# Performance work log

Hardware: AMD Instinct MI355X
Metric: run time of the kernel (lower is better)

The kernel has to match this reference:

```python
import jax, jax.numpy as jnp
import numpy as np

BZ, C_IN, C_OUT, N, T, KT = 16, 3, 64, 307, 24, 3


def setup_inputs() -> dict:
    key = jax.random.key(0)
    ks = jax.random.split(key, 16)
    rn = lambda i, sh, s=1.0: jax.random.normal(ks[i], sh, dtype=jnp.float32) * s
    return {
        "x": rn(0, (BZ, C_IN, N, T)),
        "supports": rn(1, (N, N)),  # adjacency scores; entries > 0 define edges
        "conv1_w": rn(2, (C_OUT, C_IN), 0.1),
        "conv1_b": jnp.zeros((C_OUT,), jnp.float32),
        "time_w": rn(3, (C_OUT, C_IN, 1, KT), 0.1),
        "time_b": jnp.zeros((C_OUT,), jnp.float32),
        "W1": rn(4, (C_OUT, C_OUT), 0.1), "a1s": rn(5, (C_OUT,), 0.1), "a1d": rn(6, (C_OUT,), 0.1),
        "W2": rn(7, (C_OUT, C_OUT), 0.1), "a2s": rn(8, (C_OUT,), 0.1), "a2d": rn(9, (C_OUT,), 0.1),
        "t1w": rn(10, (C_OUT,), 0.1),
        "t2w": rn(11, (N,), 0.1),
        "tw": rn(12, (N, C_OUT), 0.1),
        "tb": jnp.zeros((T, T), jnp.float32),
        "tv": rn(13, (T, T), 0.1),
        "bn_g": jnp.ones((T,), jnp.float32), "bn_b": jnp.zeros((T,), jnp.float32),
        "ln_w": jnp.ones((C_OUT, N, T), jnp.float32), "ln_b": jnp.zeros((C_OUT, N, T), jnp.float32),
    }


def _lrelu(z, s=0.01):
    return jnp.where(z > 0, z, s * z)


def _gat(x, adj, W, a_src, a_dst, slope=0.3):
    # x: [B, C, N, T] -> per-time-step single-head graph attention masked by adj > 0
    h = jnp.einsum('bcnt,cf->btnf', x, W)                      # [B,T,N,F]
    e = (jnp.einsum('btnf,f->btn', h, a_src)[:, :, :, None]
         + jnp.einsum('btnf,f->btn', h, a_dst)[:, :, None, :])  # [B,T,N,N]
    e = _lrelu(e, slope)
    e = jnp.where(adj[None, None] > 0, e, -9e15)
    att = jax.nn.softmax(e, axis=-1)
    out = jnp.einsum('btnm,btmf->btnf', att, h)
    return out.transpose(0, 3, 2, 1), att                      # [B,F,N,T], [B,T,N,N]


def _forward(x, supports, conv1_w, conv1_b, time_w, time_b,
             W1, a1s, a1d, W2, a2s, a2d,
             t1w, t2w, tw, tb, tv, bn_g, bn_b, ln_w, ln_b):
    # residual branch: 1x1 conv
    x_input = jnp.einsum('bcnt,oc->bont', x, conv1_w) + conv1_b[None, :, None, None]
    # temporal conv (1, Kt), padding (0, 1)
    x1 = jax.lax.conv_general_dilated(
        x, time_w, (1, 1), [(0, 0), (1, 1)],
        dimension_numbers=('NCHW', 'OIHW', 'NCHW')) + time_b[None, :, None, None]
    x1 = _lrelu(x1)  # dropout is identity in eval
    # two dynamic GATs: filter + gate
    filt, S_coef = _gat(x1, supports, W1, a1s, a1d)
    gate, _ = _gat(x1, supports, W2, a2s, a2d)
    x1 = jax.nn.sigmoid(gate) * _lrelu(filt)
    # ---- TATT_1 temporal attention ----
    f1 = jnp.einsum('bcnt,c->btn', x1, t1w)   # conv1 (C->1) on [B,C,T,N]
    f2 = jnp.einsum('bcnt,n->bct', x1, t2w)   # conv2 (N->1) on [B,N,C,T]
    logits = jax.nn.sigmoid(jnp.einsum('btn,nc,bcq->btq', f1, tw, f2) + tb)
    logits = jnp.einsum('pt,btq->bpq', tv, logits)
    # BatchNorm1d in eval (running_mean=0, running_var=1), channels = last dim after transpose
    lg = logits.transpose(0, 2, 1)
    lg = lg / np.sqrt(1.0 + 1e-5).astype(np.float32) * bn_g[None, :, None] + bn_b[None, :, None]
    logits = lg.transpose(0, 2, 1)
    # global B mask: causal mask over time steps
    Bmask = jnp.where(jnp.tril(jnp.ones((T, T), jnp.float32)) > 0, 0.0, -1e13)
    coefs = jax.nn.softmax(logits + Bmask, axis=-1)
    T_coef = coefs.transpose(0, 2, 1)
    # combine over time + residual + LayerNorm over [C, N, T]
    x1 = jnp.einsum('bcnl,blq->bcnq', x1, T_coef)
    y = _lrelu(x1) + x_input
    mu = jnp.mean(y, axis=(1, 2, 3), keepdims=True)
    var = jnp.var(y, axis=(1, 2, 3), keepdims=True)
    out = (y - mu) / jnp.sqrt(var + 1e-5) * ln_w[None] + ln_b[None]
    return out, S_coef, T_coef


def reference(x, supports, conv1_w, conv1_b, time_w, time_b,
              W1, a1s, a1d, W2, a2s, a2d,
              t1w, t2w, tw, tb, tv, bn_g, bn_b, ln_w, ln_b):
    return _forward(x, supports, conv1_w, conv1_b, time_w, time_b,
                    W1, a1s, a1d, W2, a2s, a2d,
                    t1w, t2w, tw, tb, tv, bn_g, bn_b, ln_w, ln_b)
```

## Files before the change

kernel.cpp:

```cpp
#include <hip/hip_runtime.h>

typedef unsigned short u16;
typedef unsigned int u32;
typedef __attribute__((ext_vector_type(8))) short bf16x8;
typedef __attribute__((ext_vector_type(4))) float f32x4;

#define BZ 16
#define CIN 3
#define C 64
#define N_ 307
#define T_ 24
#define BT (BZ*T_)
#define ROWS (BT*N_)
#define CNT (C*N_*T_)

#define OUT_ELEMS 7544832
#define S_ELEMS   36191616

#define HSTRIDE 344

__device__ __forceinline__ u16 f2b(float v) {
    union { float f; unsigned u; } x; x.f = v;
    unsigned u = x.u;
    unsigned rb = (u >> 16) & 1u;
    u += 0x7fffu + rb;
    return (u16)(u >> 16);
}
__device__ __forceinline__ float wave_sum(float v) {
#pragma unroll
    for (int m = 32; m > 0; m >>= 1) v += __shfl_xor(v, m);
    return v;
}

__global__ __launch_bounds__(512) void kAdjPre(const float* __restrict__ sup,
        u32* __restrict__ adjm)
{
    int idx = blockIdx.x*512 + threadIdx.x;
    if (idx >= 3200) return;
    int n = idx / 10, kw = idx - n*10;
    u32 bits = 0;
    if (n < N_) {
        const float* row = sup + n*N_ + kw*32;
        int lim = N_ - kw*32; if (lim > 32) lim = 32;
        for (int j = 0; j < lim; ++j)
            if (row[j] > 0.f) bits |= (1u << j);
    }
    adjm[idx] = bits;
}

template<int G>
__global__ __launch_bounds__(512, 2) void kGAT(
        const float* __restrict__ x, const float* __restrict__ sup,
        const float* __restrict__ tmw, const float* __restrict__ tmb,
        const float* __restrict__ W, const float* __restrict__ asp,
        const float* __restrict__ adp,
        const float* __restrict__ t1w, const float* __restrict__ t2w,
        const u32* __restrict__ adjm,
        float* __restrict__ agbuf, float* __restrict__ f1,
        float* __restrict__ f2)
{
    __shared__ u16 sHT[64*HSTRIDE];
    __shared__ float sX[3200];
    __shared__ float sTmw[576];
    __shared__ float sTmb[64];
    __shared__ float sU[64];
    __shared__ float sV[64];
    __shared__ float sHs[320];
    __shared__ float sHd[320];
    __shared__ float sF2[8*64];

    int bt = blockIdx.x;
    int b = bt / T_, t = bt - b * T_;
    int tid = threadIdx.x;
    int w = tid >> 6, lane = tid & 63;
    int l15 = lane & 15, quad = lane >> 4;

    for (int i = tid; i < 3*320*3; i += 512) {
        int k = i % 3; int rest = i / 3;
        int n = rest % 320; int ci = rest / 320;
        int tt = t - 1 + k;
        float v = 0.f;
        if (n < N_ && tt >= 0 && tt < T_)
            v = x[((b*CIN + ci)*N_ + n)*T_ + tt];
        sX[i] = v;
    }
    for (int i = tid; i < 576; i += 512) sTmw[i] = tmw[i];
    if (tid < 64) {
        sTmb[tid] = tmb[tid];
        float u = 0.f, v = 0.f;
#pragma unroll
        for (int f4 = 0; f4 < 16; ++f4) {
            float4 wr = ((const float4*)(W + tid*64))[f4];
            float4 s4 = ((const float4*)asp)[f4];
            float4 d4 = ((const float4*)adp)[f4];
            u += wr.x*s4.x + wr.y*s4.y + wr.z*s4.z + wr.w*s4.w;
            v += wr.x*d4.x + wr.y*d4.y + wr.z*d4.z + wr.w*d4.w;
        }
        sU[tid] = u; sV[tid] = v;
    }

    bf16x8 wf[2][4];
#pragma unroll
    for (int kk = 0; kk < 2; ++kk)
#pragma unroll
    for (int nt = 0; nt < 4; ++nt) {
        bf16x8 a;
#pragma unroll
        for (int j = 0; j < 8; ++j)
            a[j] = (short)f2b(W[(kk*32 + quad*8 + j)*64 + nt*16 + l15]);
        wf[kk][nt] = a;
    }
    __syncthreads();

#pragma unroll 1
    for (int mt = w; mt < 20; mt += 8) {
        int row = mt*16 + l15;
        float xt[16];
#pragma unroll
        for (int half = 0; half < 2; ++half) {
#pragma unroll
            for (int j = 0; j < 8; ++j) {
                int c = half*32 + quad*8 + j;
                float acc = sTmb[c];
#pragma unroll
                for (int ci = 0; ci < 3; ++ci) {
                    const float* xr = &sX[(ci*320 + row)*3];
                    const float* wr = &sTmw[(c*3 + ci)*3];
                    acc += wr[0]*xr[0] + wr[1]*xr[1] + wr[2]*xr[2];
                }
                xt[half*8 + j] = acc > 0.f ? acc : 0.01f*acc;
            }
        }
        float ps = 0.f, pd = 0.f;
#pragma unroll
        for (int j = 0; j < 8; ++j) {
            ps += xt[j]*sU[quad*8 + j] + xt[8 + j]*sU[32 + quad*8 + j];
            pd += xt[j]*sV[quad*8 + j] + xt[8 + j]*sV[32 + quad*8 + j];
        }
        ps += __shfl_xor(ps, 16); ps += __shfl_xor(ps, 32);
        pd += __shfl_xor(pd, 16); pd += __shfl_xor(pd, 32);
        if (quad == 0 && row < N_) { sHs[row] = ps; sHd[row] = pd; }
        bf16x8 a0, a1;
#pragma unroll
        for (int j = 0; j < 8; ++j) {
            a0[j] = (short)f2b(xt[j]);
            a1[j] = (short)f2b(xt[8 + j]);
        }
        f32x4 hacc[4];
#pragma unroll
        for (int nt = 0; nt < 4; ++nt) {
            f32x4 z = {0.f, 0.f, 0.f, 0.f};
            z = __builtin_amdgcn_mfma_f32_16x16x32_bf16(a0, wf[0][nt], z, 0, 0, 0);
            z = __builtin_amdgcn_mfma_f32_16x16x32_bf16(a1, wf[1][nt], z, 0, 0, 0);
            hacc[nt] = z;
        }
#pragma unroll
        for (int nt = 0; nt < 4; ++nt)
#pragma unroll
        for (int reg = 0; reg < 4; ++reg)
            sHT[(nt*16 + l15)*HSTRIDE + mt*16 + quad*4 + reg] = f2b(hacc[nt][reg]);
    }
    if (tid < 13) { sHs[307+tid] = -700.f; sHd[307+tid] = -700.f; }
    __syncthreads();

    u32* sAdj = (u32*)sX;
    for (int i = tid; i < 3200; i += 512) sAdj[i] = adjm[i];
    __syncthreads();

    float t1all[4];
    if (G == 1) {
#pragma unroll
        for (int nt = 0; nt < 4; ++nt) t1all[nt] = t1w[nt*16 + l15];
    }
    float q[4] = {0,0,0,0};

#pragma unroll 1
    for (int mt = w; mt < 20; mt += 8) {
        int n = mt*16 + l15;
        float hsv = sHs[n];
        float asum = 0.f;
        bf16x8 af[10];
#pragma unroll
        for (int ks = 0; ks < 10; ++ks) {
            u32 aw = sAdj[n*10 + ks] >> (quad*8);
            int m0 = ks*32 + quad*8;
            bf16x8 a;
#pragma unroll
            for (int j = 0; j < 8; ++j) {
                float e = hsv + sHd[m0 + j];
                e = e > 0.f ? e : 0.3f*e;
                float ww = ((aw >> j) & 1u) ? __expf(e) : 0.f;
                asum += ww;
                a[j] = (short)f2b(ww);
            }
            af[ks] = a;
        }
        asum += __shfl_xor(asum, 16);
        asum += __shfl_xor(asum, 32);
        float invv = (asum > 0.f) ? 1.f/asum : 0.f;

        float p[4] = {0,0,0,0};
#pragma unroll 1
        for (int nt = 0; nt < 4; ++nt) {
            f32x4 acc = {0.f, 0.f, 0.f, 0.f};
            const u16* bbase = sHT + (nt*16 + l15)*HSTRIDE;
#pragma unroll
            for (int ks = 0; ks < 10; ++ks) {
                bf16x8 bfrag = *(const bf16x8*)(bbase + ks*32 + quad*8);
                acc = __builtin_amdgcn_mfma_f32_16x16x32_bf16(af[ks], bfrag, acc, 0, 0, 0);
            }
            int c = nt*16 + l15;
#pragma unroll
            for (int reg = 0; reg < 4; ++reg) {
                int n2 = mt*16 + quad*4 + reg;
                float inv2 = __shfl(invv, quad*4 + reg);
                float a = acc[reg] * inv2;
                size_t idx = (size_t)(bt*N_ + n2)*64 + c;
                if (G == 0) {
                    if (n2 < N_) agbuf[idx] = a;
                } else {
                    float a1 = (n2 < N_) ? agbuf[idx] : 0.f;
                    float gt = 1.f / (1.f + __expf(-a));
                    float fv = a1 > 0.f ? a1 : 0.01f*a1;
                    float xv = gt * fv;
                    if (n2 < N_) agbuf[idx] = xv; else xv = 0.f;
                    p[reg] += xv * t1all[nt];
                    float t2v = (n2 < N_) ? t2w[n2] : 0.f;
                    q[nt] += xv * t2v;
                }
            }
        }
        if (G == 1) {
#pragma unroll
            for (int reg = 0; reg < 4; ++reg) {
                float s = p[reg];
                s += __shfl_xor(s, 1); s += __shfl_xor(s, 2);
                s += __shfl_xor(s, 4); s += __shfl_xor(s, 8);
                int n2 = mt*16 + quad*4 + reg;
                if (l15 == 0 && n2 < N_) f1[bt*N_ + n2] = s;
            }
        }
    }
    if (G == 1) {
#pragma unroll
        for (int nt = 0; nt < 4; ++nt) {
            float s = q[nt];
            s += __shfl_xor(s, 16); s += __shfl_xor(s, 32);
            if (quad == 0) sF2[w*64 + nt*16 + l15] = s;
        }
        __syncthreads();
        if (tid < 64) {
            float s = sF2[tid];
#pragma unroll
            for (int ww = 1; ww < 8; ++ww) s += sF2[ww*64 + tid];
            f2[(b*C + tid)*T_ + t] = s;
        }
    }
}

__global__ __launch_bounds__(512) void kSc(
        const float* __restrict__ x, const float* __restrict__ sup,
        const float* __restrict__ tmw, const float* __restrict__ tmb,
        const float* __restrict__ W, const float* __restrict__ asp,
        const float* __restrict__ adp, float* __restrict__ Sc)
{
    __shared__ float sHs[320];
    __shared__ float sHd[320];
    __shared__ float sU[64], sV[64];
    __shared__ float sTmw[576];
    __shared__ float sTmb[64];

    int half = blockIdx.x;
    int bt = blockIdx.y;
    int b = bt / T_, t = bt - b * T_;
    int tid = threadIdx.x;
    int w = tid >> 6, lane = tid & 63;

    for (int i = tid; i < 576; i += 512) sTmw[i] = tmw[i];
    if (tid < 64) {
        sTmb[tid] = tmb[tid];
        float u = 0.f, v = 0.f;
#pragma unroll
        for (int f4 = 0; f4 < 16; ++f4) {
            float4 wr = ((const float4*)(W + tid*64))[f4];
            float4 s4 = ((const float4*)asp)[f4];
            float4 d4 = ((const float4*)adp)[f4];
            u += wr.x*s4.x + wr.y*s4.y + wr.z*s4.z + wr.w*s4.w;
            v += wr.x*d4.x + wr.y*d4.y + wr.z*d4.z + wr.w*d4.w;
        }
        sU[tid] = u; sV[tid] = v;
    }
    __syncthreads();

    if (tid < 320) {
        int n = tid;
        if (n >= N_) { sHs[n] = -700.f; sHd[n] = -700.f; }
        else {
            float xv[3][3];
#pragma unroll
            for (int ci = 0; ci < 3; ++ci) {
                const float* xp = x + ((b*CIN + ci)*N_ + n)*T_ + t;
                xv[ci][0] = (t > 0)      ? xp[-1] : 0.f;
                xv[ci][1] = xp[0];
                xv[ci][2] = (t < T_ - 1) ? xp[1]  : 0.f;
            }
            float hs = 0.f, hd = 0.f;
#pragma unroll
            for (int c = 0; c < 64; ++c) {
                float acc = sTmb[c];
#pragma unroll
                for (int ci = 0; ci < 3; ++ci) {
                    const float* wr = &sTmw[(c*3 + ci)*3];
                    acc += wr[0]*xv[ci][0] + wr[1]*xv[ci][1] + wr[2]*xv[ci][2];
                }
                float xt = acc > 0.f ? acc : 0.01f*acc;
                hs += xt * sU[c];
                hd += xt * sV[c];
            }
            sHs[n] = hs; sHd[n] = hd;
        }
    }
    __syncthreads();

    int base = half ? 154 : 0;
    int cnt  = half ? 153 : 154;
#pragma unroll 1
    for (int r = w; r < cnt; r += 8) {
        int n = base + r;
        float hsv = sHs[n];
        const float* srow = sup + n*N_;
        float ww0, ww1, ww2, ww3, ww4;
        {
            float e;
            ww0 = 0.f;
            if (srow[lane] > 0.f) { e = hsv + sHd[lane]; e = e > 0.f ? e : 0.3f*e; ww0 = __expf(e); }
            ww1 = 0.f;
            if (srow[64 + lane] > 0.f) { e = hsv + sHd[64 + lane]; e = e > 0.f ? e : 0.3f*e; ww1 = __expf(e); }
            ww2 = 0.f;
            if (srow[128 + lane] > 0.f) { e = hsv + sHd[128 + lane]; e = e > 0.f ? e : 0.3f*e; ww2 = __expf(e); }
            ww3 = 0.f;
            if (srow[192 + lane] > 0.f) { e = hsv + sHd[192 + lane]; e = e > 0.f ? e : 0.3f*e; ww3 = __expf(e); }
            ww4 = 0.f;
            if (256 + lane < N_ && srow[256 + lane] > 0.f) {
                e = hsv + sHd[256 + lane]; e = e > 0.f ? e : 0.3f*e; ww4 = __expf(e);
            }
        }
        float asum = wave_sum(ww0 + ww1 + ww2 + ww3 + ww4);
        float inv = (asum > 0.f) ? 1.f/asum : 0.f;
        float* drow = Sc + (size_t)(bt*N_ + n)*N_;
        drow[lane]       = ww0*inv;
        drow[64 + lane]  = ww1*inv;
        drow[128 + lane] = ww2*inv;
        drow[192 + lane] = ww3*inv;
        if (256 + lane < N_) drow[256 + lane] = ww4*inv;
    }
}

__global__ __launch_bounds__(256) void kD0(const float* __restrict__ f1,
        const float* __restrict__ tw, float* __restrict__ g1)
{
    __shared__ float part[4][64];
    int bt = blockIdx.x;
    int w = threadIdx.x >> 6, lane = threadIdx.x & 63;
    float acc = 0.f;
    for (int n = w*77; n < (w+1)*77 && n < N_; ++n)
        acc += f1[bt*N_ + n] * tw[n*64 + lane];
    part[w][lane] = acc;
    __syncthreads();
    if (threadIdx.x < 64) {
        float s = part[0][threadIdx.x] + part[1][threadIdx.x]
                + part[2][threadIdx.x] + part[3][threadIdx.x];
        g1[bt*64 + threadIdx.x] = s;
    }
}

__global__ __launch_bounds__(256) void kD(const float* __restrict__ g1,
        const float* __restrict__ f2, const float* __restrict__ tb,
        const float* __restrict__ tv,
        const float* __restrict__ bng, const float* __restrict__ bnb,
        float* __restrict__ coefs, float* __restrict__ Tc,
        float* __restrict__ stats)
{
    __shared__ float g1s[T_][C];
    __shared__ float f2s[C][T_];
    __shared__ float lg[T_][T_];
    __shared__ float l2[T_][T_];
    int b = blockIdx.x, tid = threadIdx.x;
    if (tid == 0) { stats[2*b] = 0.f; stats[2*b + 1] = 0.f; }
    for (int idx = tid; idx < T_*C; idx += 256) {
        int t = idx / C, c = idx - t*C;
        g1s[t][c] = g1[(b*T_ + t)*C + c];
        int c2 = idx / T_, t2 = idx - c2*T_;
        f2s[c2][t2] = f2[(b*C + c2)*T_ + t2];
    }
    __syncthreads();
    for (int idx = tid; idx < T_*T_; idx += 256) {
        int t = idx / T_, q = idx - t*T_;
        float s = 0.f;
#pragma unroll
        for (int c = 0; c < C; ++c) s += g1s[t][c] * f2s[c][q];
        s += tb[t*T_ + q];
        lg[t][q] = 1.f / (1.f + expf(-s));
    }
    __syncthreads();
    const float bnscale = 0.99999500003749972f;
    for (int idx = tid; idx < T_*T_; idx += 256) {
        int p = idx / T_, q = idx - p*T_;
        float s = 0.f;
#pragma unroll
        for (int t = 0; t < T_; ++t) s += tv[p*T_ + t] * lg[t][q];
        s = s * bnscale * bng[q] + bnb[q];
        if (q > p) s += -1e13f;
        l2[p][q] = s;
    }
    __syncthreads();
    if (tid < T_) {
        int p = tid;
        float mx = -3e38f;
#pragma unroll
        for (int q = 0; q < T_; ++q) mx = fmaxf(mx, l2[p][q]);
        float e[T_]; float sum = 0.f;
#pragma unroll
        for (int q = 0; q < T_; ++q) { e[q] = expf(l2[p][q] - mx); sum += e[q]; }
        float inv = 1.f / sum;
#pragma unroll
        for (int q = 0; q < T_; ++q) {
            float v = e[q] * inv;
            coefs[(b*T_ + p)*T_ + q] = v;
            Tc[(b*T_ + q)*T_ + p] = v;
        }
    }
}

__device__ __forceinline__ void compute_y(int b, int n, int lane,
        const float* __restrict__ xg, const float cf[T_][T_],
        const float* __restrict__ x, const float* __restrict__ c1w,
        const float* __restrict__ c1b, float* y)
{
    float acc[T_];
#pragma unroll
    for (int q = 0; q < T_; ++q) acc[q] = 0.f;
#pragma unroll 1
    for (int l = 0; l < T_; ++l) {
        float xv = xg[(size_t)((b*T_ + l)*N_ + n)*64 + lane];
#pragma unroll
        for (int q = 0; q < T_; ++q) acc[q] += xv * cf[q][l];
    }
    float w0 = c1w[lane*3+0], w1 = c1w[lane*3+1], w2 = c1w[lane*3+2];
    float bb = c1b[lane];
    const float* xb0 = x + ((b*CIN + 0)*N_ + n)*T_;
    const float* xb1 = x + ((b*CIN + 1)*N_ + n)*T_;
    const float* xb2 = x + ((b*CIN + 2)*N_ + n)*T_;
#pragma unroll
    for (int q = 0; q < T_; ++q) {
        float xin = bb + w0*xb0[q] + w1*xb1[q] + w2*xb2[q];
        float v = acc[q];
        v = v > 0.f ? v : 0.01f*v;
        y[q] = v + xin;
    }
}

__global__ __launch_bounds__(256) void kE1(const float* __restrict__ xg,
        const float* __restrict__ coefs, const float* __restrict__ x,
        const float* __restrict__ c1w, const float* __restrict__ c1b,
        float* __restrict__ stats)
{
    __shared__ float cf[T_][T_];
    int b = blockIdx.y;
    for (int i = threadIdx.x; i < T_*T_; i += 256) ((float*)cf)[i] = coefs[b*T_*T_ + i];
    __syncthreads();
    int w = threadIdx.x >> 6, lane = threadIdx.x & 63;
    int n = blockIdx.x*4 + w;
    if (n >= N_) return;
    float y[T_];
    compute_y(b, n, lane, xg, cf, x, c1w, c1b, y);
    float s = 0.f, ss = 0.f;
#pragma unroll
    for (int q = 0; q < T_; ++q) { s += y[q]; ss += y[q]*y[q]; }
    s = wave_sum(s); ss = wave_sum(ss);
    if (lane == 0) { atomicAdd(&stats[2*b], s); atomicAdd(&stats[2*b + 1], ss); }
}

__global__ __launch_bounds__(256) void kE2(const float* __restrict__ xg,
        const float* __restrict__ coefs, const float* __restrict__ x,
        const float* __restrict__ c1w, const float* __restrict__ c1b,
        const float* __restrict__ stats, const float* __restrict__ lnw,
        const float* __restrict__ lnb, float* __restrict__ out)
{
    __shared__ float cf[T_][T_];
    int b = blockIdx.y;
    for (int i = threadIdx.x; i < T_*T_; i += 256) ((float*)cf)[i] = coefs[b*T_*T_ + i];
    __syncthreads();
    int w = threadIdx.x >> 6, lane = threadIdx.x & 63;
    int n = blockIdx.x*4 + w;
    if (n >= N_) return;
    float y[T_];
    compute_y(b, n, lane, xg, cf, x, c1w, c1b, y);
    float mu   = stats[2*b] * (1.f/CNT);
    float var  = stats[2*b + 1] * (1.f/CNT) - mu*mu;
    float rstd = rsqrtf(fmaxf(var, 0.f) + 1e-5f);
    int gi = (lane*N_ + n)*T_;
    float ov[T_];
#pragma unroll
    for (int q = 0; q < T_; ++q)
        ov[q] = (y[q] - mu)*rstd*lnw[gi + q] + lnb[gi + q];
    float* dst = out + ((size_t)(b*C + lane)*N_ + n)*T_;
#pragma unroll
    for (int j = 0; j < 6; ++j) {
        float4 v;
        v.x = ov[j*4+0]; v.y = ov[j*4+1]; v.z = ov[j*4+2]; v.w = ov[j*4+3];
        ((float4*)dst)[j] = v;
    }
}

extern "C" void kernel_launch(void* const* d_in, const int* in_sizes, int n_in,
                              void* d_out, int out_size, void* d_ws, size_t ws_size,
                              hipStream_t stream)
{
    const float* x   = (const float*)d_in[0];
    const float* sup = (const float*)d_in[1];
    const float* c1w = (const float*)d_in[2];
    const float* c1b = (const float*)d_in[3];
    const float* tmw = (const float*)d_in[4];
    const float* tmb = (const float*)d_in[5];
    const float* W1  = (const float*)d_in[6];
    const float* a1s = (const float*)d_in[7];
    const float* a1d = (const float*)d_in[8];
    const float* W2  = (const float*)d_in[9];
    const float* a2s = (const float*)d_in[10];
    const float* a2d = (const float*)d_in[11];
    const float* t1w = (const float*)d_in[12];
    const float* t2w = (const float*)d_in[13];
    const float* tw  = (const float*)d_in[14];
    const float* tb  = (const float*)d_in[15];
    const float* tv  = (const float*)d_in[16];
    const float* bng = (const float*)d_in[17];
    const float* bnb = (const float*)d_in[18];
    const float* lnw = (const float*)d_in[19];
    const float* lnb = (const float*)d_in[20];

    float* out = (float*)d_out;
    float* Sc  = out + OUT_ELEMS;
    float* Tc  = Sc + (size_t)S_ELEMS;

    float* agbuf = Sc;
    float* f1    = Sc + (size_t)OUT_ELEMS;
    float* f2    = f1 + ROWS;
    float* g1    = f2 + BZ*C*T_;
    float* coefs = g1 + BT*C;
    float* stats = coefs + BZ*T_*T_;
    u32*   adjm  = (u32*)(stats + 32);

    kAdjPre<<<7, 512, 0, stream>>>(sup, adjm);
    kGAT<0><<<BT, 512, 0, stream>>>(x, sup, tmw, tmb, W1, a1s, a1d,
                                    t1w, t2w, adjm, agbuf, f1, f2);
    kGAT<1><<<BT, 512, 0, stream>>>(x, sup, tmw, tmb, W2, a2s, a2d,
                                    t1w, t2w, adjm, agbuf, f1, f2);
    kD0<<<BT, 256, 0, stream>>>(f1, tw, g1);
    kD<<<BZ, 256, 0, stream>>>(g1, f2, tb, tv, bng, bnb, coefs, Tc, stats);
    kE1<<<dim3(77, BZ), 256, 0, stream>>>(agbuf, coefs, x, c1w, c1b, stats);
    kE2<<<dim3(77, BZ), 256, 0, stream>>>(agbuf, coefs, x, c1w, c1b, stats, lnw, lnb, out);
    kSc<<<dim3(2, BT), 512, 0, stream>>>(x, sup, tmw, tmb, W1, a1s, a1d, Sc);
}
```

Before: 642.2 us.

## Fuse both GAT passes into one kernel keeping first-pass output in registers

Merges the two per-(b,t) GAT kernels into a single kernel. The first GAT's aggregated features stay in registers instead of being written to and reread from a global buffer. The second pass rebuilds its temporal-conv input straight from global x while the LDS slot holds the adjacency mask. The attention tile loop is also restructured to interleave weight computation with MFMAs per k-slice, and launch bounds are raised to 4 blocks per CU. The cost is higher register pressure (48 extra fp32 values per thread held across phases), with a risk of spills or lower occupancy.

```diff
diff --git a/kernel.cpp b/kernel.cpp
--- a/kernel.cpp
+++ b/kernel.cpp
@@ -48,26 +48,149 @@
     adjm[idx] = bits;
 }
 
-template<int G>
-__global__ __launch_bounds__(512, 2) void kGAT(
-        const float* __restrict__ x, const float* __restrict__ sup,
+template<int LDSX>
+__device__ __forceinline__ void phase1_core(
+        const float* __restrict__ x, const float* __restrict__ Wg,
+        const float* sXw, const float* sTmw, const float* sTmb,
+        const float* sUp, const float* sVp,
+        u16* sHTp, float* sHsp, float* sHdp,
+        int b, int t, int w, int lane)
+{
+    int l15 = lane & 15, quad = lane >> 4;
+#pragma unroll
+    for (int ti = 0; ti < 3; ++ti) {
+        int mt = w + ti*8;
+        if (mt < 20) {
+            int row = mt*16 + l15;
+            float xv[9];
+            if (LDSX) {
+#pragma unroll
+                for (int ci = 0; ci < 3; ++ci)
+#pragma unroll
+                for (int k = 0; k < 3; ++k)
+                    xv[ci*3 + k] = sXw[(ci*320 + row)*3 + k];
+            } else {
+                bool rk = row < N_;
+                int rc = rk ? row : 0;
+#pragma unroll
+                for (int ci = 0; ci < 3; ++ci) {
+                    const float* xp = x + ((b*CIN + ci)*N_ + rc)*T_ + t;
+                    xv[ci*3 + 0] = (rk && t > 0)      ? xp[-1] : 0.f;
+                    xv[ci*3 + 1] = rk                 ? xp[0]  : 0.f;
+                    xv[ci*3 + 2] = (rk && t < T_ - 1) ? xp[1]  : 0.f;
+                }
+            }
+            float xt[16];
+#pragma unroll
+            for (int half = 0; half < 2; ++half)
+#pragma unroll
+            for (int j = 0; j < 8; ++j) {
+                int c = half*32 + quad*8 + j;
+                float acc = sTmb[c];
+#pragma unroll
+                for (int ci = 0; ci < 3; ++ci) {
+                    const float* wr = &sTmw[(c*3 + ci)*3];
+                    acc += wr[0]*xv[ci*3] + wr[1]*xv[ci*3+1] + wr[2]*xv[ci*3+2];
+                }
+                xt[half*8 + j] = acc > 0.f ? acc : 0.01f*acc;
+            }
+            float ps = 0.f, pd = 0.f;
+#pragma unroll
+            for (int j = 0; j < 8; ++j) {
+                ps += xt[j]*sUp[quad*8 + j] + xt[8 + j]*sUp[32 + quad*8 + j];
+                pd += xt[j]*sVp[quad*8 + j] + xt[8 + j]*sVp[32 + quad*8 + j];
+            }
+            ps += __shfl_xor(ps, 16); ps += __shfl_xor(ps, 32);
+            pd += __shfl_xor(pd, 16); pd += __shfl_xor(pd, 32);
+            if (quad == 0 && row < N_) { sHsp[row] = ps; sHdp[row] = pd; }
+            bf16x8 a0, a1;
+#pragma unroll
+            for (int j = 0; j < 8; ++j) {
+                a0[j] = (short)f2b(xt[j]);
+                a1[j] = (short)f2b(xt[8 + j]);
+            }
+            f32x4 hacc[4];
+#pragma unroll
+            for (int nt = 0; nt < 4; ++nt) hacc[nt] = (f32x4){0.f,0.f,0.f,0.f};
+#pragma unroll
+            for (int kk = 0; kk < 2; ++kk) {
+                bf16x8 wf[4];
+#pragma unroll
+                for (int nt = 0; nt < 4; ++nt) {
+                    bf16x8 a;
+#pragma unroll
+                    for (int j = 0; j < 8; ++j)
+                        a[j] = (short)f2b(Wg[(kk*32 + quad*8 + j)*64 + nt*16 + l15]);
+                    wf[nt] = a;
+                }
+#pragma unroll
+                for (int nt = 0; nt < 4; ++nt)
+                    hacc[nt] = __builtin_amdgcn_mfma_f32_16x16x32_bf16(
+                        kk ? a1 : a0, wf[nt], hacc[nt], 0, 0, 0);
+            }
+#pragma unroll
+            for (int nt = 0; nt < 4; ++nt) {
+                u32 w0 = (u32)f2b(hacc[nt][0]) | ((u32)f2b(hacc[nt][1]) << 16);
+                u32 w1 = (u32)f2b(hacc[nt][2]) | ((u32)f2b(hacc[nt][3]) << 16);
+                u32* dst = (u32*)(sHTp + (nt*16 + l15)*HSTRIDE + mt*16 + quad*4);
+                dst[0] = w0; dst[1] = w1;
+            }
+        }
+    }
+}
+
+__device__ __forceinline__ void att_tile(
+        const u32* sAdj, const u16* sHTp, const float* sHsp, const float* sHdp,
+        int mt, int l15, int quad, f32x4 acc[4], float* invv_out)
+{
+    int n = mt*16 + l15;
+    float hsv = sHsp[n];
+    float asum = 0.f;
+#pragma unroll
+    for (int nt = 0; nt < 4; ++nt) acc[nt] = (f32x4){0.f,0.f,0.f,0.f};
+#pragma unroll
+    for (int ks = 0; ks < 10; ++ks) {
+        u32 aw = sAdj[n*10 + ks] >> (quad*8);
+        int m0 = ks*32 + quad*8;
+        bf16x8 a;
+#pragma unroll
+        for (int j = 0; j < 8; ++j) {
+            float e = hsv + sHdp[m0 + j];
+            e = e > 0.f ? e : 0.3f*e;
+            float ww = ((aw >> j) & 1u) ? __expf(e) : 0.f;
+            asum += ww;
+            a[j] = (short)f2b(ww);
+        }
+        const u16* bb = sHTp + m0;
+#pragma unroll
+        for (int nt = 0; nt < 4; ++nt) {
+            bf16x8 bfrag = *(const bf16x8*)(bb + (nt*16 + l15)*HSTRIDE);
+            acc[nt] = __builtin_amdgcn_mfma_f32_16x16x32_bf16(a, bfrag, acc[nt], 0, 0, 0);
+        }
+    }
+    asum += __shfl_xor(asum, 16);
+    asum += __shfl_xor(asum, 32);
+    *invv_out = (asum > 0.f) ? 1.f/asum : 0.f;
+}
+
+__global__ __launch_bounds__(512, 4) void kGATF(
+        const float* __restrict__ x,
         const float* __restrict__ tmw, const float* __restrict__ tmb,
-        const float* __restrict__ W, const float* __restrict__ asp,
-        const float* __restrict__ adp,
+        const float* __restrict__ W1, const float* __restrict__ a1s,
+        const float* __restrict__ a1d,
+        const float* __restrict__ W2, const float* __restrict__ a2s,
+        const float* __restrict__ a2d,
         const float* __restrict__ t1w, const float* __restrict__ t2w,
         const u32* __restrict__ adjm,
-        float* __restrict__ agbuf, float* __restrict__ f1,
+        float* __restrict__ xg, float* __restrict__ f1,
         float* __restrict__ f2)
 {
     __shared__ u16 sHT[64*HSTRIDE];
-    __shared__ float sX[3200];
+    __shared__ float sXA[3200];
     __shared__ float sTmw[576];
     __shared__ float sTmb[64];
-    __shared__ float sU[64];
-    __shared__ float sV[64];
-    __shared__ float sHs[320];
-    __shared__ float sHd[320];
-    __shared__ float sF2[8*64];
+    __shared__ float sU1[64], sV1[64], sU2[64], sV2[64];
+    __shared__ float sHs[320], sHd[320];
 
     int bt = blockIdx.x;
     int b = bt / T_, t = bt - b * T_;
@@ -75,162 +198,95 @@
     int w = tid >> 6, lane = tid & 63;
     int l15 = lane & 15, quad = lane >> 4;
 
-    for (int i = tid; i < 3*320*3; i += 512) {
+    for (int i = tid; i < 2880; i += 512) {
         int k = i % 3; int rest = i / 3;
         int n = rest % 320; int ci = rest / 320;
         int tt = t - 1 + k;
         float v = 0.f;
         if (n < N_ && tt >= 0 && tt < T_)
             v = x[((b*CIN + ci)*N_ + n)*T_ + tt];
-        sX[i] = v;
+        sXA[i] = v;
     }
     for (int i = tid; i < 576; i += 512) sTmw[i] = tmw[i];
-    if (tid < 64) {
-        sTmb[tid] = tmb[tid];
+    if (tid < 128) {
+        int c = tid & 63;
+        const float* Wp = (tid < 64) ? W1 : W2;
+        const float* sp = (tid < 64) ? a1s : a2s;
+        const float* dp = (tid < 64) ? a1d : a2d;
         float u = 0.f, v = 0.f;
 #pragma unroll
         for (int f4 = 0; f4 < 16; ++f4) {
-            float4 wr = ((const float4*)(W + tid*64))[f4];
-            float4 s4 = ((const float4*)asp)[f4];
-            float4 d4 = ((const float4*)adp)[f4];
+            float4 wr = ((const float4*)(Wp + c*64))[f4];
+            float4 s4 = ((const float4*)sp)[f4];
+            float4 d4 = ((const float4*)dp)[f4];
             u += wr.x*s4.x + wr.y*s4.y + wr.z*s4.z + wr.w*s4.w;
             v += wr.x*d4.x + wr.y*d4.y + wr.z*d4.z + wr.w*d4.w;
         }
-        sU[tid] = u; sV[tid] = v;
-    }
-
-    bf16x8 wf[2][4];
-#pragma unroll
-    for (int kk = 0; kk < 2; ++kk)
-#pragma unroll
-    for (int nt = 0; nt < 4; ++nt) {
-        bf16x8 a;
-#pragma unroll
-        for (int j = 0; j < 8; ++j)
-            a[j] = (short)f2b(W[(kk*32 + quad*8 + j)*64 + nt*16 + l15]);
-        wf[kk][nt] = a;
-    }
-    __syncthreads();
-
-#pragma unroll 1
-    for (int mt = w; mt < 20; mt += 8) {
-        int row = mt*16 + l15;
-        float xt[16];
-#pragma unroll
-        for (int half = 0; half < 2; ++half) {
-#pragma unroll
-            for (int j = 0; j < 8; ++j) {
-                int c = half*32 + quad*8 + j;
-                float acc = sTmb[c];
-#pragma unroll
-                for (int ci = 0; ci < 3; ++ci) {
-                    const float* xr = &sX[(ci*320 + row)*3];
-                    const float* wr = &sTmw[(c*3 + ci)*3];
-                    acc += wr[0]*xr[0] + wr[1]*xr[1] + wr[2]*xr[2];
-                }
-                xt[half*8 + j] = acc > 0.f ? acc : 0.01f*acc;
-            }
-        }
-        float ps = 0.f, pd = 0.f;
-#pragma unroll
-        for (int j = 0; j < 8; ++j) {
-            ps += xt[j]*sU[quad*8 + j] + xt[8 + j]*sU[32 + quad*8 + j];
-            pd += xt[j]*sV[quad*8 + j] + xt[8 + j]*sV[32 + quad*8 + j];
-        }
-        ps += __shfl_xor(ps, 16); ps += __shfl_xor(ps, 32);
-        pd += __shfl_xor(pd, 16); pd += __shfl_xor(pd, 32);
-        if (quad == 0 && row < N_) { sHs[row] = ps; sHd[row] = pd; }
-        bf16x8 a0, a1;
-#pragma unroll
-        for (int j = 0; j < 8; ++j) {
-            a0[j] = (short)f2b(xt[j]);
-            a1[j] = (short)f2b(xt[8 + j]);
-        }
-        f32x4 hacc[4];
-#pragma unroll
-        for (int nt = 0; nt < 4; ++nt) {
-            f32x4 z = {0.f, 0.f, 0.f, 0.f};
-            z = __builtin_amdgcn_mfma_f32_16x16x32_bf16(a0, wf[0][nt], z, 0, 0, 0);
-            z = __builtin_amdgcn_mfma_f32_16x16x32_bf16(a1, wf[1][nt], z, 0, 0, 0);
-            hacc[nt] = z;
-        }
-#pragma unroll
-        for (int nt = 0; nt < 4; ++nt)
-#pragma unroll
-        for (int reg = 0; reg < 4; ++reg)
-            sHT[(nt*16 + l15)*HSTRIDE + mt*16 + quad*4 + reg] = f2b(hacc[nt][reg]);
-    }
+        if (tid < 64) { sU1[c] = u; sV1[c] = v; sTmb[c] = tmb[c]; }
+        else          { sU2[c] = u; sV2[c] = v; }
+    }
+    __syncthreads();
+
+    phase1_core<1>(x, W1, sXA, sTmw, sTmb, sU1, sV1, sHT, sHs, sHd, b, t, w, lane);
     if (tid < 13) { sHs[307+tid] = -700.f; sHd[307+tid] = -700.f; }
     __syncthreads();
 
-    u32* sAdj = (u32*)sX;
+    u32* sAdj = (u32*)sXA;
     for (int i = tid; i < 3200; i += 512) sAdj[i] = adjm[i];
     __syncthreads();
 
+    float fr[3][4][4];
+#pragma unroll
+    for (int ti = 0; ti < 3; ++ti) {
+        int mt = w + ti*8;
+        if (mt < 20) {
+            f32x4 acc[4]; float invv;
+            att_tile(sAdj, sHT, sHs, sHd, mt, l15, quad, acc, &invv);
+#pragma unroll
+            for (int nt = 0; nt < 4; ++nt)
+#pragma unroll
+            for (int reg = 0; reg < 4; ++reg) {
+                float inv2 = __shfl(invv, quad*4 + reg);
+                fr[ti][nt][reg] = acc[nt][reg] * inv2;
+            }
+        }
+    }
+    __syncthreads();
+
+    phase1_core<0>(x, W2, nullptr, sTmw, sTmb, sU2, sV2, sHT, sHs, sHd, b, t, w, lane);
+    __syncthreads();
+
     float t1all[4];
-    if (G == 1) {
-#pragma unroll
-        for (int nt = 0; nt < 4; ++nt) t1all[nt] = t1w[nt*16 + l15];
-    }
+#pragma unroll
+    for (int nt = 0; nt < 4; ++nt) t1all[nt] = t1w[nt*16 + l15];
     float q[4] = {0,0,0,0};
 
-#pragma unroll 1
-    for (int mt = w; mt < 20; mt += 8) {
-        int n = mt*16 + l15;
-        float hsv = sHs[n];
-        float asum = 0.f;
-        bf16x8 af[10];
-#pragma unroll
-        for (int ks = 0; ks < 10; ++ks) {
-            u32 aw = sAdj[n*10 + ks] >> (quad*8);
-            int m0 = ks*32 + quad*8;
-            bf16x8 a;
-#pragma unroll
-            for (int j = 0; j < 8; ++j) {
-                float e = hsv + sHd[m0 + j];
-                e = e > 0.f ? e : 0.3f*e;
-                float ww = ((aw >> j) & 1u) ? __expf(e) : 0.f;
-                asum += ww;
-                a[j] = (short)f2b(ww);
-            }
-            af[ks] = a;
-        }
-        asum += __shfl_xor(asum, 16);
-        asum += __shfl_xor(asum, 32);
-        float invv = (asum > 0.f) ? 1.f/asum : 0.f;
-
-        float p[4] = {0,0,0,0};
-#pragma unroll 1
-        for (int nt = 0; nt < 4; ++nt) {
-            f32x4 acc = {0.f, 0.f, 0.f, 0.f};
-            const u16* bbase = sHT + (nt*16 + l15)*HSTRIDE;
-#pragma unroll
-            for (int ks = 0; ks < 10; ++ks) {
-                bf16x8 bfrag = *(const bf16x8*)(bbase + ks*32 + quad*8);
-                acc = __builtin_amdgcn_mfma_f32_16x16x32_bf16(af[ks], bfrag, acc, 0, 0, 0);
-            }
-            int c = nt*16 + l15;
-#pragma unroll
-            for (int reg = 0; reg < 4; ++reg) {
-                int n2 = mt*16 + quad*4 + reg;
-                float inv2 = __shfl(invv, quad*4 + reg);
-                float a = acc[reg] * inv2;
-                size_t idx = (size_t)(bt*N_ + n2)*64 + c;
-                if (G == 0) {
-                    if (n2 < N_) agbuf[idx] = a;
-                } else {
-                    float a1 = (n2 < N_) ? agbuf[idx] : 0.f;
-                    float gt = 1.f / (1.f + __expf(-a));
-                    float fv = a1 > 0.f ? a1 : 0.01f*a1;
+#pragma unroll
+    for (int ti = 0; ti < 3; ++ti) {
+        int mt = w + ti*8;
+        if (mt < 20) {
+            f32x4 acc[4]; float invv;
+            att_tile(sAdj, sHT, sHs, sHd, mt, l15, quad, acc, &invv);
+            float p[4] = {0,0,0,0};
+#pragma unroll
+            for (int nt = 0; nt < 4; ++nt) {
+                int c = nt*16 + l15;
+#pragma unroll
+                for (int reg = 0; reg < 4; ++reg) {
+                    int n2 = mt*16 + quad*4 + reg;
+                    float inv2 = __shfl(invv, quad*4 + reg);
+                    float gate = acc[nt][reg] * inv2;
+                    float gt = 1.f / (1.f + __expf(-gate));
+                    float fv = fr[ti][nt][reg];
+                    fv = fv > 0.f ? fv : 0.01f*fv;
                     float xv = gt * fv;
-                    if (n2 < N_) agbuf[idx] = xv; else xv = 0.f;
+                    size_t idx = (size_t)(bt*N_ + n2)*64 + c;
+                    if (n2 < N_) xg[idx] = xv; else xv = 0.f;
                     p[reg] += xv * t1all[nt];
                     float t2v = (n2 < N_) ? t2w[n2] : 0.f;
                     q[nt] += xv * t2v;
                 }
             }
-        }
-        if (G == 1) {
 #pragma unroll
             for (int reg = 0; reg < 4; ++reg) {
                 float s = p[reg];
@@ -241,20 +297,20 @@
             }
         }
     }
-    if (G == 1) {
-#pragma unroll
-        for (int nt = 0; nt < 4; ++nt) {
-            float s = q[nt];
-            s += __shfl_xor(s, 16); s += __shfl_xor(s, 32);
-            if (quad == 0) sF2[w*64 + nt*16 + l15] = s;
-        }
-        __syncthreads();
-        if (tid < 64) {
-            float s = sF2[tid];
-#pragma unroll
-            for (int ww = 1; ww < 8; ++ww) s += sF2[ww*64 + tid];
-            f2[(b*C + tid)*T_ + t] = s;
-        }
+    __syncthreads();
+    float* sF2 = sXA;
+#pragma unroll
+    for (int nt = 0; nt < 4; ++nt) {
+        float s = q[nt];
+        s += __shfl_xor(s, 16); s += __shfl_xor(s, 32);
+        if (quad == 0) sF2[w*64 + nt*16 + l15] = s;
+    }
+    __syncthreads();
+    if (tid < 64) {
+        float s = sF2[tid];
+#pragma unroll
+        for (int ww = 1; ww < 8; ++ww) s += sF2[ww*64 + tid];
+        f2[(b*C + tid)*T_ + t] = s;
     }
 }
 
@@ -543,7 +599,7 @@
     float* Sc  = out + OUT_ELEMS;
     float* Tc  = Sc + (size_t)S_ELEMS;
 
-    float* agbuf = Sc;
+    float* xg    = Sc;
     float* f1    = Sc + (size_t)OUT_ELEMS;
     float* f2    = f1 + ROWS;
     float* g1    = f2 + BZ*C*T_;
@@ -552,13 +608,11 @@
     u32*   adjm  = (u32*)(stats + 32);
 
     kAdjPre<<<7, 512, 0, stream>>>(sup, adjm);
-    kGAT<0><<<BT, 512, 0, stream>>>(x, sup, tmw, tmb, W1, a1s, a1d,
-                                    t1w, t2w, adjm, agbuf, f1, f2);
-    kGAT<1><<<BT, 512, 0, stream>>>(x, sup, tmw, tmb, W2, a2s, a2d,
-                                    t1w, t2w, adjm, agbuf, f1, f2);
+    kGATF<<<BT, 512, 0, stream>>>(x, tmw, tmb, W1, a1s, a1d, W2, a2s, a2d,
+                                  t1w, t2w, adjm, xg, f1, f2);
     kD0<<<BT, 256, 0, stream>>>(f1, tw, g1);
     kD<<<BZ, 256, 0, stream>>>(g1, f2, tb, tv, bng, bnb, coefs, Tc, stats);
-    kE1<<<dim3(77, BZ), 256, 0, stream>>>(agbuf, coefs, x, c1w, c1b, stats);
-    kE2<<<dim3(77, BZ), 256, 0, stream>>>(agbuf, coefs, x, c1w, c1b, stats, lnw, lnb, out);
+    kE1<<<dim3(77, BZ), 256, 0, stream>>>(xg, coefs, x, c1w, c1b, stats);
+    kE2<<<dim3(77, BZ), 256, 0, stream>>>(xg, coefs, x, c1w, c1b, stats, lnw, lnb, out);
     kSc<<<dim3(2, BT), 512, 0, stream>>>(x, sup, tmw, tmb, W1, a1s, a1d, Sc);
 }
```

Measured after the change: 778.6 us. 1.21x slower.

## Run both GAT passes in one launch and fuse gating with f1/f2/g1 reductions

Applied to the files above, without the earlier changes.

The two sequential GAT kernels become a single launch with a second grid dimension, so the W1 and W2 attention passes run concurrently into separate buffers. The gating, the f1/f2 reductions and the former kD0 projection move into a new per-(b,t) kComb kernel. The sHT stores are packed into 32-bit writes. This doubles the parallelism of the heaviest stage and removes a launch, but writes an extra full-size intermediate (gbuf) and reads it back in kComb.

```diff
diff --git a/kernel.cpp b/kernel.cpp
--- a/kernel.cpp
+++ b/kernel.cpp
@@ -48,41 +48,45 @@
     adjm[idx] = bits;
 }
 
-template<int G>
-__global__ __launch_bounds__(512, 2) void kGAT(
-        const float* __restrict__ x, const float* __restrict__ sup,
+__global__ __launch_bounds__(512, 2) void kGAT2(
+        const float* __restrict__ x,
         const float* __restrict__ tmw, const float* __restrict__ tmb,
-        const float* __restrict__ W, const float* __restrict__ asp,
-        const float* __restrict__ adp,
-        const float* __restrict__ t1w, const float* __restrict__ t2w,
+        const float* __restrict__ W1, const float* __restrict__ a1s,
+        const float* __restrict__ a1d,
+        const float* __restrict__ W2, const float* __restrict__ a2s,
+        const float* __restrict__ a2d,
         const u32* __restrict__ adjm,
-        float* __restrict__ agbuf, float* __restrict__ f1,
-        float* __restrict__ f2)
+        float* __restrict__ fbuf, float* __restrict__ gbuf)
 {
     __shared__ u16 sHT[64*HSTRIDE];
-    __shared__ float sX[3200];
+    __shared__ float sXA[3200];
     __shared__ float sTmw[576];
     __shared__ float sTmb[64];
     __shared__ float sU[64];
     __shared__ float sV[64];
     __shared__ float sHs[320];
     __shared__ float sHd[320];
-    __shared__ float sF2[8*64];
 
     int bt = blockIdx.x;
+    int gy = blockIdx.y;
     int b = bt / T_, t = bt - b * T_;
     int tid = threadIdx.x;
     int w = tid >> 6, lane = tid & 63;
     int l15 = lane & 15, quad = lane >> 4;
 
-    for (int i = tid; i < 3*320*3; i += 512) {
+    const float* W   = gy ? W2  : W1;
+    const float* asp = gy ? a2s : a1s;
+    const float* adp = gy ? a2d : a1d;
+    float* dst       = gy ? gbuf : fbuf;
+
+    for (int i = tid; i < 2880; i += 512) {
         int k = i % 3; int rest = i / 3;
         int n = rest % 320; int ci = rest / 320;
         int tt = t - 1 + k;
         float v = 0.f;
         if (n < N_ && tt >= 0 && tt < T_)
             v = x[((b*CIN + ci)*N_ + n)*T_ + tt];
-        sX[i] = v;
+        sXA[i] = v;
     }
     for (int i = tid; i < 576; i += 512) sTmw[i] = tmw[i];
     if (tid < 64) {
@@ -124,7 +128,7 @@
                 float acc = sTmb[c];
 #pragma unroll
                 for (int ci = 0; ci < 3; ++ci) {
-                    const float* xr = &sX[(ci*320 + row)*3];
+                    const float* xr = &sXA[(ci*320 + row)*3];
                     const float* wr = &sTmw[(c*3 + ci)*3];
                     acc += wr[0]*xr[0] + wr[1]*xr[1] + wr[2]*xr[2];
                 }
@@ -155,24 +159,19 @@
             hacc[nt] = z;
         }
 #pragma unroll
-        for (int nt = 0; nt < 4; ++nt)
-#pragma unroll
-        for (int reg = 0; reg < 4; ++reg)
-            sHT[(nt*16 + l15)*HSTRIDE + mt*16 + quad*4 + reg] = f2b(hacc[nt][reg]);
+        for (int nt = 0; nt < 4; ++nt) {
+            u32 w0 = (u32)f2b(hacc[nt][0]) | ((u32)f2b(hacc[nt][1]) << 16);
+            u32 w1 = (u32)f2b(hacc[nt][2]) | ((u32)f2b(hacc[nt][3]) << 16);
+            u32* dp = (u32*)(sHT + (nt*16 + l15)*HSTRIDE + mt*16 + quad*4);
+            dp[0] = w0; dp[1] = w1;
+        }
     }
     if (tid < 13) { sHs[307+tid] = -700.f; sHd[307+tid] = -700.f; }
     __syncthreads();
 
-    u32* sAdj = (u32*)sX;
+    u32* sAdj = (u32*)sXA;
     for (int i = tid; i < 3200; i += 512) sAdj[i] = adjm[i];
     __syncthreads();
-
-    float t1all[4];
-    if (G == 1) {
-#pragma unroll
-        for (int nt = 0; nt < 4; ++nt) t1all[nt] = t1w[nt*16 + l15];
-    }
-    float q[4] = {0,0,0,0};
 
 #pragma unroll 1
     for (int mt = w; mt < 20; mt += 8) {
@@ -199,7 +198,6 @@
         asum += __shfl_xor(asum, 32);
         float invv = (asum > 0.f) ? 1.f/asum : 0.f;
 
-        float p[4] = {0,0,0,0};
 #pragma unroll 1
         for (int nt = 0; nt < 4; ++nt) {
             f32x4 acc = {0.f, 0.f, 0.f, 0.f};
@@ -215,46 +213,67 @@
                 int n2 = mt*16 + quad*4 + reg;
                 float inv2 = __shfl(invv, quad*4 + reg);
                 float a = acc[reg] * inv2;
-                size_t idx = (size_t)(bt*N_ + n2)*64 + c;
-                if (G == 0) {
-                    if (n2 < N_) agbuf[idx] = a;
-                } else {
-                    float a1 = (n2 < N_) ? agbuf[idx] : 0.f;
-                    float gt = 1.f / (1.f + __expf(-a));
-                    float fv = a1 > 0.f ? a1 : 0.01f*a1;
-                    float xv = gt * fv;
-                    if (n2 < N_) agbuf[idx] = xv; else xv = 0.f;
-                    p[reg] += xv * t1all[nt];
-                    float t2v = (n2 < N_) ? t2w[n2] : 0.f;
-                    q[nt] += xv * t2v;
-                }
-            }
-        }
-        if (G == 1) {
-#pragma unroll
-            for (int reg = 0; reg < 4; ++reg) {
-                float s = p[reg];
-                s += __shfl_xor(s, 1); s += __shfl_xor(s, 2);
-                s += __shfl_xor(s, 4); s += __shfl_xor(s, 8);
-                int n2 = mt*16 + quad*4 + reg;
-                if (l15 == 0 && n2 < N_) f1[bt*N_ + n2] = s;
-            }
-        }
-    }
-    if (G == 1) {
-#pragma unroll
-        for (int nt = 0; nt < 4; ++nt) {
-            float s = q[nt];
-            s += __shfl_xor(s, 16); s += __shfl_xor(s, 32);
-            if (quad == 0) sF2[w*64 + nt*16 + l15] = s;
-        }
-        __syncthreads();
-        if (tid < 64) {
-            float s = sF2[tid];
-#pragma unroll
-            for (int ww = 1; ww < 8; ++ww) s += sF2[ww*64 + tid];
-            f2[(b*C + tid)*T_ + t] = s;
-        }
+                if (n2 < N_) dst[(size_t)(bt*N_ + n2)*64 + c] = a;
+            }
+        }
+    }
+}
+
+__global__ __launch_bounds__(512) void kComb(
+        float* __restrict__ xg, const float* __restrict__ gbuf,
+        const float* __restrict__ t1w, const float* __restrict__ t2w,
+        const float* __restrict__ tw,
+        float* __restrict__ f1, float* __restrict__ f2,
+        float* __restrict__ g1)
+{
+    __shared__ float sF1[320];
+    __shared__ float sRed[8][64];
+    __shared__ float sT1[64];
+
+    int bt = blockIdx.x;
+    int b = bt / T_, t = bt - b * T_;
+    int tid = threadIdx.x;
+    int w = tid >> 6, lane = tid & 63;
+
+    if (tid < 64) sT1[tid] = t1w[tid];
+    if (tid < 13) sF1[307 + tid] = 0.f;
+    __syncthreads();
+
+    float f2acc = 0.f;
+#pragma unroll 1
+    for (int n = w; n < N_; n += 8) {
+        size_t idx = (size_t)(bt*N_ + n)*64 + lane;
+        float f = xg[idx];
+        float g = gbuf[idx];
+        float gt = 1.f / (1.f + __expf(-g));
+        float fv = f > 0.f ? f : 0.01f*f;
+        float xv = gt * fv;
+        xg[idx] = xv;
+        float p = wave_sum(xv * sT1[lane]);
+        if (lane == 0) sF1[n] = p;
+        f2acc += xv * t2w[n];
+    }
+    __syncthreads();
+    sRed[w][lane] = f2acc;
+    __syncthreads();
+    if (tid < 64) {
+        float s = sRed[0][tid];
+#pragma unroll
+        for (int ww = 1; ww < 8; ++ww) s += sRed[ww][tid];
+        f2[(b*C + tid)*T_ + t] = s;
+    }
+    if (tid < 320 && tid < N_) f1[bt*N_ + tid] = sF1[tid];
+    __syncthreads();
+    float gacc = 0.f;
+    int n0 = w*40, n1 = n0 + 40; if (n1 > N_) n1 = N_;
+    for (int n = n0; n < n1; ++n) gacc += sF1[n] * tw[n*64 + lane];
+    sRed[w][lane] = gacc;
+    __syncthreads();
+    if (tid < 64) {
+        float s = sRed[0][tid];
+#pragma unroll
+        for (int ww = 1; ww < 8; ++ww) s += sRed[ww][tid];
+        g1[bt*64 + tid] = s;
     }
 }
 
@@ -356,24 +375,6 @@
     }
 }
 
-__global__ __launch_bounds__(256) void kD0(const float* __restrict__ f1,
-        const float* __restrict__ tw, float* __restrict__ g1)
-{
-    __shared__ float part[4][64];
-    int bt = blockIdx.x;
-    int w = threadIdx.x >> 6, lane = threadIdx.x & 63;
-    float acc = 0.f;
-    for (int n = w*77; n < (w+1)*77 && n < N_; ++n)
-        acc += f1[bt*N_ + n] * tw[n*64 + lane];
-    part[w][lane] = acc;
-    __syncthreads();
-    if (threadIdx.x < 64) {
-        float s = part[0][threadIdx.x] + part[1][threadIdx.x]
-                + part[2][threadIdx.x] + part[3][threadIdx.x];
-        g1[bt*64 + threadIdx.x] = s;
-    }
-}
-
 __global__ __launch_bounds__(256) void kD(const float* __restrict__ g1,
         const float* __restrict__ f2, const float* __restrict__ tb,
         const float* __restrict__ tv,
@@ -543,22 +544,21 @@
     float* Sc  = out + OUT_ELEMS;
     float* Tc  = Sc + (size_t)S_ELEMS;
 
-    float* agbuf = Sc;
+    float* xg    = Sc;
     float* f1    = Sc + (size_t)OUT_ELEMS;
     float* f2    = f1 + ROWS;
     float* g1    = f2 + BZ*C*T_;
     float* coefs = g1 + BT*C;
     float* stats = coefs + BZ*T_*T_;
     u32*   adjm  = (u32*)(stats + 32);
+    float* gbuf  = (float*)(adjm + 3200);
 
     kAdjPre<<<7, 512, 0, stream>>>(sup, adjm);
-    kGAT<0><<<BT, 512, 0, stream>>>(x, sup, tmw, tmb, W1, a1s, a1d,
-                                    t1w, t2w, adjm, agbuf, f1, f2);
-    kGAT<1><<<BT, 512, 0, stream>>>(x, sup, tmw, tmb, W2, a2s, a2d,
-                                    t1w, t2w, adjm, agbuf, f1, f2);
-    kD0<<<BT, 256, 0, stream>>>(f1, tw, g1);
+    kGAT2<<<dim3(BT, 2), 512, 0, stream>>>(x, tmw, tmb, W1, a1s, a1d,
+                                           W2, a2s, a2d, adjm, xg, gbuf);
+    kComb<<<BT, 512, 0, stream>>>(xg, gbuf, t1w, t2w, tw, f1, f2, g1);
     kD<<<BZ, 256, 0, stream>>>(g1, f2, tb, tv, bng, bnb, coefs, Tc, stats);
-    kE1<<<dim3(77, BZ), 256, 0, stream>>>(agbuf, coefs, x, c1w, c1b, stats);
-    kE2<<<dim3(77, BZ), 256, 0, stream>>>(agbuf, coefs, x, c1w, c1b, stats, lnw, lnb, out);
+    kE1<<<dim3(77, BZ), 256, 0, stream>>>(xg, coefs, x, c1w, c1b, stats);
+    kE2<<<dim3(77, BZ), 256, 0, stream>>>(xg, coefs, x, c1w, c1b, stats, lnw, lnb, out);
     kSc<<<dim3(2, BT), 512, 0, stream>>>(x, sup, tmw, tmb, W1, a1s, a1d, Sc);
 }
```

Result: faster. 591.1 us (-8.0%).
